# Performance work log

Hardware: AMD Instinct MI355X
Metric: run time of the kernel (lower is better)

Reference implementation:

```python
import jax, jax.numpy as jnp
import numpy as np
from jax import lax

WINDOW_SIZE = 9
MAX_DISP = 192
RADIUS = WINDOW_SIZE // 2


def setup_inputs() -> dict:
    key = jax.random.key(0)
    k1, k2, k3 = jax.random.split(key, 3)
    B, H, W = 2, 256, 512
    left_img = jax.random.uniform(k1, (B, 1, H, W), dtype=jnp.float32)
    right_img = jax.random.uniform(k2, (B, 1, H, W), dtype=jnp.float32)
    target_disp = jax.random.randint(k3, (B, 1, H, W), 0, MAX_DISP).astype(jnp.float32)
    return {"left_img": left_img, "right_img": right_img, "target_disp": target_disp}


def _census_transform(img):
    # img: [B,1,H,W] -> census bits: [B, ws*ws-1, H-2r, W-2r]
    # (original allocates ws*ws channels but leaves the center-slot channel
    #  all-zero; it contributes 0 to the hamming sum, so we omit it.)
    B, _, H, W = img.shape
    Hc, Wc = H - 2 * RADIUS, W - 2 * RADIUS
    center = img[:, :, RADIUS:RADIUS + Hc, RADIUS:RADIUS + Wc]
    chans = []
    for i in range(WINDOW_SIZE):
        for j in range(WINDOW_SIZE):
            if i == RADIUS and j == RADIUS:
                continue
            win = img[:, :, i:i + Hc, j:j + Wc]
            chans.append((win > center).astype(jnp.float32))
    return jnp.concatenate(chans, axis=1)  # [B, 80, Hc, Wc]


def _cost_volume(left_census, right_census):
    # hamming cost per disparity via scan (one [B,1,Hc,Wc] slice at a time)
    Wc = left_census.shape[-1]
    w_base = jnp.arange(Wc)

    def step(carry, d):
        widx = w_base + d
        valid = (widx < Wc)[None, None, None, :]
        rc_d = jnp.where(valid,
                         right_census[..., jnp.clip(widx, 0, Wc - 1)],
                         jnp.float32(0))
        cost = jnp.sum(jnp.abs(left_census - rc_d), axis=1, keepdims=True)
        return carry, cost  # [B,1,Hc,Wc]

    _, costs = lax.scan(step, None, jnp.arange(MAX_DISP))  # [D,B,1,Hc,Wc]
    return jnp.moveaxis(costs, 0, 2)  # [B,1,D,Hc,Wc]


def reference(left_img, right_img, target_disp):
    lc = _census_transform(left_img)
    rc = _census_transform(right_img)
    cost_volume = _cost_volume(lc, rc)  # [B,1,D,Hc,Wc]

    disp_crop = target_disp[:, :, RADIUS:-RADIUS, RADIUS:-RADIUS]  # [B,1,Hc,Wc]
    tidx = jnp.clip(disp_crop.astype(jnp.int32), 0, MAX_DISP - 1)
    # gather cost at target disparity per pixel
    best_cost = jnp.take_along_axis(cost_volume, tidx[:, :, None], axis=2)[:, :, 0]
    mask = (disp_crop > 0).astype(jnp.float32)
    valid_pixels = jnp.sum(mask) + 1e-6
    return jnp.sum(best_cost * mask) / valid_pixels
```

## Files before the change

### kernel.cpp

```cpp
#include <hip/hip_runtime.h>

constexpr int RADIUS   = 4;
constexpr int MAX_DISP = 192;
constexpr int B  = 2;
constexpr int H  = 256;
constexpr int W  = 512;
constexpr int Hc = H - 2 * RADIUS;
constexpr int Wc = W - 2 * RADIUS;

constexpr int BLOCK = 256;
constexpr int ROWS  = B * Hc;
constexpr int TX    = 4;
constexpr int TPR   = Wc / TX;

constexpr unsigned long long INVALID_MASK = 0xFFFF0000FFFF0000ull;

__device__ __forceinline__ unsigned long long
row_partial(const float* __restrict__ left,
            const float* __restrict__ right,
            const float* __restrict__ disp,
            ulonglong2* rbuf, uint2* red, int bid) {
    const int b   = bid / Hc;
    const int y   = bid % Hc;
    const int tid = threadIdx.x;
    const bool isRight = (tid < 128);
    const int t   = tid & 127;
    const int x0  = t * TX;

    unsigned long long lo[TX] = {0,0,0,0};
    unsigned long long hi[TX] = {0,0,0,0};

    if (t < TPR) {
        const float* img  = isRight ? right : left;
        const float* base = img + ((size_t)b * H + y) * W + x0;

        const float4 c4 = *(const float4*)(base + 4 * W + 4);
        const float ctr[TX] = { c4.x, c4.y, c4.z, c4.w };

        #pragma unroll
        for (int r = 0; r < 9; ++r) {
            const float4* p = (const float4*)(base + r * W);
            const float4 a = p[0], m = p[1], cc = p[2];
            const float f[12] = { a.x,a.y,a.z,a.w, m.x,m.y,m.z,m.w,
                                  cc.x,cc.y,cc.z,cc.w };
            #pragma unroll
            for (int j = 0; j < 9; ++j) {
                if (r == 4 && j == 4) continue;
                const int bit = r * 9 + j;
                #pragma unroll
                for (int q = 0; q < TX; ++q) {
                    const unsigned long long tb = (f[q + j] > ctr[q]) ? 1ull : 0ull;
                    if (bit < 64) lo[q] |= tb << bit;
                    else          hi[q] |= tb << (bit - 64);
                }
            }
        }
        if (isRight) {
            #pragma unroll
            for (int q = 0; q < TX; ++q) {
                ulonglong2 v; v.x = lo[q]; v.y = hi[q];
                rbuf[x0 + q] = v;
            }
        }
    }
    __syncthreads();

    unsigned int cost = 0, cnt = 0;
    if (!isRight && t < TPR) {
        const float4 d4 = *(const float4*)(disp + ((size_t)b * H + y + RADIUS) * W
                                                + x0 + RADIUS);
        const float dv[TX] = { d4.x, d4.y, d4.z, d4.w };
        #pragma unroll
        for (int q = 0; q < TX; ++q) {
            if (dv[q] > 0.0f) {
                ++cnt;
                const int x = x0 + q;
                const int d = min((int)dv[q], MAX_DISP - 1);
                if (x + d < Wc) {
                    const ulonglong2 R = rbuf[x + d];
                    cost += (unsigned int)(__popcll(lo[q] ^ R.x) +
                                           __popcll(hi[q] ^ R.y));
                } else {
                    cost += (unsigned int)(__popcll(lo[q]) + __popcll(hi[q]));
                }
            }
        }
    }

    #pragma unroll
    for (int off = 32; off > 0; off >>= 1) {
        cost += __shfl_down(cost, off);
        cnt  += __shfl_down(cnt,  off);
    }
    const int wave = tid >> 6;
    if ((tid & 63) == 0) red[wave] = make_uint2(cost, cnt);
    __syncthreads();

    unsigned int c = 0, n = 0;
    if (tid == 0) {
        #pragma unroll
        for (int w = 0; w < BLOCK / 64; ++w) { c += red[w].x; n += red[w].y; }
    }
    return ((unsigned long long)c << 32) | n;
}

__global__ __launch_bounds__(BLOCK)
void fused_single_kernel(const float* __restrict__ left,
                         const float* __restrict__ right,
                         const float* __restrict__ disp,
                         unsigned long long* __restrict__ partials,
                         float* __restrict__ out) {
    __shared__ ulonglong2 rbuf[Wc];
    __shared__ uint2 red[BLOCK / 64];

    const int bid = blockIdx.x;
    if (bid < ROWS) {
        const unsigned long long packed =
            row_partial(left, right, disp, rbuf, red, bid);
        if (threadIdx.x == 0)
            __hip_atomic_store(&partials[bid], packed,
                               __ATOMIC_RELAXED, __HIP_MEMORY_SCOPE_AGENT);
        return;
    }

    unsigned int c = 0, n = 0;
    for (int i = threadIdx.x; i < ROWS; i += BLOCK) {
        unsigned long long p;
        for (;;) {
            p = __hip_atomic_load(&partials[i], __ATOMIC_RELAXED,
                                  __HIP_MEMORY_SCOPE_AGENT);
            if ((p & INVALID_MASK) == 0ull) break;
            __builtin_amdgcn_s_sleep(1);
        }
        c += (unsigned int)(p >> 32);
        n += (unsigned int)(p & 0xffffffffu);
    }
    #pragma unroll
    for (int off = 32; off > 0; off >>= 1) {
        c += __shfl_down(c, off);
        n += __shfl_down(n, off);
    }
    const int wave = threadIdx.x >> 6;
    if ((threadIdx.x & 63) == 0) red[wave] = make_uint2(c, n);
    __syncthreads();
    if (threadIdx.x == 0) {
        unsigned int tc = 0, tn = 0;
        #pragma unroll
        for (int w = 0; w < BLOCK / 64; ++w) { tc += red[w].x; tn += red[w].y; }
        out[0] = (float)tc / ((float)tn + 1e-6f);
    }
}

extern "C" void kernel_launch(void* const* d_in, const int* in_sizes, int n_in,
                              void* d_out, int out_size, void* d_ws, size_t ws_size,
                              hipStream_t stream) {
    const float* left  = (const float*)d_in[0];
    const float* right = (const float*)d_in[1];
    const float* disp  = (const float*)d_in[2];
    float* out = (float*)d_out;
    unsigned long long* partials = (unsigned long long*)d_ws;

    fused_single_kernel<<<ROWS + 1, BLOCK, 0, stream>>>(left, right, disp,
                                                        partials, out);
}
```

Before: 64.90 us.

## Split census window rows across two blocks per image row

Each image row is now handled by two producer blocks. One computes the census bits for window rows 0-4 and the other for rows 5-8, so each fits in a single 64-bit word and the Hamming cost is summed per half. This doubles the grid, halves the per-thread compare/shift work and register use, and shrinks the shared buffer to 64-bit entries. The disparity load is hoisted ahead of the census work. The cost is redundant disparity loads and center loads per half, twice as many partials for the consumer block to spin on, and more launch blocks.

```diff
diff --git a/kernel.cpp b/kernel.cpp
--- a/kernel.cpp
+++ b/kernel.cpp
@@ -8,81 +8,86 @@
 constexpr int Hc = H - 2 * RADIUS;
 constexpr int Wc = W - 2 * RADIUS;
 
-constexpr int BLOCK = 256;
-constexpr int ROWS  = B * Hc;
-constexpr int TX    = 4;
-constexpr int TPR   = Wc / TX;
+constexpr int BLOCK     = 256;
+constexpr int ROWSETS   = B * Hc;
+constexpr int PRODUCERS = 2 * ROWSETS;
+constexpr int TX        = 4;
+constexpr int TPR       = Wc / TX;
 
 constexpr unsigned long long INVALID_MASK = 0xFFFF0000FFFF0000ull;
 
+template<int R0, int R1>
+__device__ __forceinline__ void
+census_bits(const float* __restrict__ base, const float ctr[TX],
+            unsigned long long cw[TX]) {
+    #pragma unroll
+    for (int r = R0; r < R1; ++r) {
+        const float4* p = (const float4*)(base + r * W);
+        const float4 a = p[0], m = p[1], cc = p[2];
+        const float f[12] = { a.x,a.y,a.z,a.w, m.x,m.y,m.z,m.w,
+                              cc.x,cc.y,cc.z,cc.w };
+        #pragma unroll
+        for (int j = 0; j < 9; ++j) {
+            if (r == 4 && j == 4) continue;
+            const int bit = (r - R0) * 9 + j;
+            #pragma unroll
+            for (int q = 0; q < TX; ++q) {
+                const unsigned long long tb = (f[q + j] > ctr[q]) ? 1ull : 0ull;
+                cw[q] |= tb << bit;
+            }
+        }
+    }
+}
+
 __device__ __forceinline__ unsigned long long
-row_partial(const float* __restrict__ left,
-            const float* __restrict__ right,
-            const float* __restrict__ disp,
-            ulonglong2* rbuf, uint2* red, int bid) {
-    const int b   = bid / Hc;
-    const int y   = bid % Hc;
-    const int tid = threadIdx.x;
+half_partial(const float* __restrict__ left,
+             const float* __restrict__ right,
+             const float* __restrict__ disp,
+             unsigned long long* rbuf, uint2* red, int bid) {
+    const int row  = bid >> 1;
+    const int half = bid & 1;
+    const int b    = row / Hc;
+    const int y    = row % Hc;
+    const int tid  = threadIdx.x;
     const bool isRight = (tid < 128);
-    const int t   = tid & 127;
-    const int x0  = t * TX;
+    const int t    = tid & 127;
+    const int x0   = t * TX;
+    const bool active = (t < TPR);
 
-    unsigned long long lo[TX] = {0,0,0,0};
-    unsigned long long hi[TX] = {0,0,0,0};
+    float dv[TX] = {0.f, 0.f, 0.f, 0.f};
+    if (!isRight && active) {
+        const float4 d4 = *(const float4*)(disp + ((size_t)b * H + y + RADIUS) * W
+                                                + x0 + RADIUS);
+        dv[0] = d4.x; dv[1] = d4.y; dv[2] = d4.z; dv[3] = d4.w;
+    }
 
-    if (t < TPR) {
+    unsigned long long cw[TX] = {0ull, 0ull, 0ull, 0ull};
+    if (active) {
         const float* img  = isRight ? right : left;
         const float* base = img + ((size_t)b * H + y) * W + x0;
 
         const float4 c4 = *(const float4*)(base + 4 * W + 4);
         const float ctr[TX] = { c4.x, c4.y, c4.z, c4.w };
 
+        if (half == 0) census_bits<0, 5>(base, ctr, cw);
+        else           census_bits<5, 9>(base, ctr, cw);
+    }
+    if (isRight && active) {
         #pragma unroll
-        for (int r = 0; r < 9; ++r) {
-            const float4* p = (const float4*)(base + r * W);
-            const float4 a = p[0], m = p[1], cc = p[2];
-            const float f[12] = { a.x,a.y,a.z,a.w, m.x,m.y,m.z,m.w,
-                                  cc.x,cc.y,cc.z,cc.w };
-            #pragma unroll
-            for (int j = 0; j < 9; ++j) {
-                if (r == 4 && j == 4) continue;
-                const int bit = r * 9 + j;
-                #pragma unroll
-                for (int q = 0; q < TX; ++q) {
-                    const unsigned long long tb = (f[q + j] > ctr[q]) ? 1ull : 0ull;
-                    if (bit < 64) lo[q] |= tb << bit;
-                    else          hi[q] |= tb << (bit - 64);
-                }
-            }
-        }
-        if (isRight) {
-            #pragma unroll
-            for (int q = 0; q < TX; ++q) {
-                ulonglong2 v; v.x = lo[q]; v.y = hi[q];
-                rbuf[x0 + q] = v;
-            }
-        }
+        for (int q = 0; q < TX; ++q) rbuf[x0 + q] = cw[q];
     }
     __syncthreads();
 
     unsigned int cost = 0, cnt = 0;
-    if (!isRight && t < TPR) {
-        const float4 d4 = *(const float4*)(disp + ((size_t)b * H + y + RADIUS) * W
-                                                + x0 + RADIUS);
-        const float dv[TX] = { d4.x, d4.y, d4.z, d4.w };
+    if (!isRight && active) {
         #pragma unroll
         for (int q = 0; q < TX; ++q) {
             if (dv[q] > 0.0f) {
-                ++cnt;
+                if (half == 0) ++cnt;
                 const int x = x0 + q;
                 const int d = min((int)dv[q], MAX_DISP - 1);
-                if (x + d < Wc) {
-                    const ulonglong2 R = rbuf[x + d];
-                    cost += (unsigned int)(__popcll(lo[q] ^ R.x) +
-                                           __popcll(hi[q] ^ R.y));
-                } else {
-                    cost += (unsigned int)(__popcll(lo[q]) + __popcll(hi[q]));
-                }
+                const unsigned long long r64 = (x + d < Wc) ? rbuf[x + d] : 0ull;
+                cost += (unsigned int)__popcll(cw[q] ^ r64);
             }
         }
     }
@@ -110,13 +115,13 @@
                          const float* __restrict__ disp,
                          unsigned long long* __restrict__ partials,
                          float* __restrict__ out) {
-    __shared__ ulonglong2 rbuf[Wc];
+    __shared__ unsigned long long rbuf[Wc];
     __shared__ uint2 red[BLOCK / 64];
 
     const int bid = blockIdx.x;
-    if (bid < ROWS) {
+    if (bid < PRODUCERS) {
         const unsigned long long packed =
-            row_partial(left, right, disp, rbuf, red, bid);
+            half_partial(left, right, disp, rbuf, red, bid);
         if (threadIdx.x == 0)
             __hip_atomic_store(&partials[bid], packed,
                                __ATOMIC_RELAXED, __HIP_MEMORY_SCOPE_AGENT);
@@ -124,7 +129,7 @@
     }
 
     unsigned int c = 0, n = 0;
-    for (int i = threadIdx.x; i < ROWS; i += BLOCK) {
+    for (int i = threadIdx.x; i < PRODUCERS; i += BLOCK) {
         unsigned long long p;
         for (;;) {
             p = __hip_atomic_load(&partials[i], __ATOMIC_RELAXED,
@@ -160,6 +165,6 @@
     float* out = (float*)d_out;
     unsigned long long* partials = (unsigned long long*)d_ws;
 
-    fused_single_kernel<<<ROWS + 1, BLOCK, 0, stream>>>(left, right, disp,
-                                                        partials, out);
+    fused_single_kernel<<<PRODUCERS + 1, BLOCK, 0, stream>>>(left, right, disp,
+                                                             partials, out);
 }
```

New measurement: 65.24 us. Within noise of the previous version (+0.5%).
